# Optimization experiments

Hardware: AMD Instinct MI355X
Metric: run time of the kernel (lower is better)

Reference implementation:

```python
import math
import jax, jax.numpy as jnp
import numpy as np

# ---- SLAYER neuron / simulation constants (from config) ----
THETA = 10.0      # spike threshold
TAU_SR = 10.0     # PSP (SRM) kernel time constant
TAU_REF = 1.0     # refractory kernel time constant
TS = 1.0          # simulation time step
T_SAMPLE = 500    # number of time bins
B, N_IN, N_HID, N_OUT = 64, 1024, 1024, 10


def _alpha_kernel(tau, mult, eps=0.01):
    """slayer _calculateAlphaKernel: mult * t/tau * exp(1 - t/tau), truncated."""
    vals = []
    t = 0.0
    while t < T_SAMPLE:
        v = mult * t / tau * math.exp(1.0 - t / tau)
        if abs(v) < eps and t > tau:
            break
        vals.append(v)
        t += TS
    return np.asarray(vals, np.float32)

SRM_KERNEL = jnp.asarray(_alpha_kernel(TAU_SR, 1.0))            # [K]
REF_KERNEL = jnp.asarray(_alpha_kernel(TAU_REF, -2.0 * THETA))  # [Kr], REF_KERNEL[0] == 0


def dense(x, W):
    # per-timestep fully-connected layer (slayer.dense == 1x1x1 conv3d, no bias)
    # x: [B, Nin, T], W: [Nout, Nin] -> [B, Nout, T]
    return jnp.einsum('oi,bit->bot', W, x)


def psp(x):
    # causal temporal convolution with the SRM kernel: out[t] = Ts * sum_k srm[k] * x[t-k]
    Bx, N, T = x.shape
    K = SRM_KERNEL.shape[0]
    k = SRM_KERNEL[::-1].reshape(1, 1, K).astype(x.dtype)  # flip -> true convolution
    y = jax.lax.conv_general_dilated(
        x.reshape(Bx * N, 1, T), k, (1,), [(K - 1, 0)],
        dimension_numbers=('NCH', 'OIH', 'NCH'))
    return y.reshape(Bx, N, T) * TS


def spike_impl(u_in):
    # sequential LIF thresholding with refractory feedback (slayer spike kernel)
    # u_in: [B, N, T] membrane drive; returns (spikes, membrane) both [B, N, T]
    Kr = REF_KERNEL.shape[0]
    # buf[j] is the refractory contribution arriving at step t+j; new spike at t
    # contributes REF_KERNEL[j] at t+j (REF_KERNEL[0]==0), i.e. shifted kernel into buf.
    refk = jnp.concatenate([REF_KERNEL[1:], jnp.zeros((1,), u_in.dtype)]).astype(u_in.dtype)
    buf0 = jnp.zeros(u_in.shape[:-1] + (Kr,), u_in.dtype)

    def step(buf, u_t):
        u = u_t + buf[..., 0]                              # membrane at time t
        s = (u >= THETA).astype(u_in.dtype) / TS           # spike (amplitude 1/Ts)
        buf = jnp.concatenate([buf[..., 1:], jnp.zeros_like(buf[..., :1])], axis=-1)
        buf = buf + s[..., None] * refk
        return buf, (s, u)

    _, (s, u) = jax.lax.scan(step, buf0, jnp.moveaxis(u_in, -1, 0))
    return jnp.moveaxis(s, 0, -1), jnp.moveaxis(u, 0, -1)


def setup_inputs() -> dict:
    key = jax.random.key(0)
    k1, k2, k3 = jax.random.split(key, 3)
    spike_input = (jax.random.uniform(k1, (B, N_IN, T_SAMPLE)) < 0.05).astype(jnp.float32)
    W1 = jax.random.normal(k2, (N_HID, N_IN), jnp.float32) * 0.3
    W2 = jax.random.normal(k3, (N_OUT, N_HID), jnp.float32) * 0.3
    return {"spike_input": spike_input, "W1": W1, "W2": W2}


def reference(spike_input, W1, W2):
    s1, _ = spike_impl(psp(dense(spike_input, W1)))
    s2, _ = spike_impl(psp(dense(s1, W2)))
    return s2
```

## Files before the change

kernel.cpp:

```cpp
#include <hip/hip_runtime.h>
#include <stdint.h>
#include <math.h>

#define T_SIM 500
#define NB    64
#define NIN   1024
#define NHID  1024
#define NOUT  10
#define KSRM  77
#define CHUNK 32
#define TT5   12
#define NT5   42
#define RING5 128

__device__ __forceinline__ double srm_tap(int k) {
  double u = (double)k / 10.0;
  double v = u * exp(1.0 - u);
  return (double)(float)v;
}
__device__ __forceinline__ double ref_tap(int j) {
  double v = (-20.0 * (double)j) * exp(1.0 - (double)j);
  return (double)(float)v;
}

__global__ __launch_bounds__(64)
void k_pack(const float* __restrict__ x, unsigned long long* __restrict__ bits) {
  const int b = blockIdx.x, ig = blockIdx.y, tc = blockIdx.z;
  const int lane = threadIdx.x;
  const float* xr = x + ((size_t)b * NIN + ig * 64 + lane) * T_SIM;
  const int t0 = tc * 100;
  for (int t = t0; t < t0 + 100; t += 4) {
    const float4 v = *(const float4*)(xr + t);
    unsigned long long m0 = __ballot(v.x > 0.5f);
    unsigned long long m1 = __ballot(v.y > 0.5f);
    unsigned long long m2 = __ballot(v.z > 0.5f);
    unsigned long long m3 = __ballot(v.w > 0.5f);
    if (lane == 0) {
      unsigned long long* w = bits + (size_t)(b * T_SIM + t) * 16 + ig;
      w[0] = m0; w[16] = m1; w[32] = m2; w[48] = m3;
    }
  }
}

__global__ __launch_bounds__(256)
void k_transpose(const float* __restrict__ W1, float* __restrict__ W1T) {
  __shared__ float tile[64][65];
  const int bo = blockIdx.x * 64, bi = blockIdx.y * 64;
  for (int k = threadIdx.x; k < 4096; k += 256) {
    int r = k >> 6, c = k & 63;
    tile[r][c] = W1[(size_t)(bo + r) * NIN + bi + c];
  }
  __syncthreads();
  for (int k = threadIdx.x; k < 4096; k += 256) {
    int r = k >> 6, c = k & 63;
    W1T[(size_t)(bi + r) * NHID + bo + c] = tile[c][r];
  }
}

__global__ __launch_bounds__(128)
void k_dense1(const uint32_t* __restrict__ bits, const float* __restrict__ W1T,
              double* __restrict__ a1c, int col_base) {
  __shared__ int list[NIN];
  __shared__ int nact_s;
  const int col_loc = blockIdx.x;
  const int tid = threadIdx.x;
  if (tid < 32) {
    uint32_t w = bits[(size_t)(col_base + col_loc) * 32 + tid];
    int c = __popc(w);
    int p = c;
#pragma unroll
    for (int d = 1; d < 32; d <<= 1) {
      int q = __shfl_up(p, d);
      if (tid >= d) p += q;
    }
    int excl = p - c;
    while (w) {
      const int j = __ffs(w) - 1;
      w &= w - 1;
      list[excl++] = tid * 32 + j;
    }
    if (tid == 31) nact_s = excl;
  }
  __syncthreads();
  const int n = nact_s;
  const int o = blockIdx.y * 512 + tid * 4;
  double ax[4] = {0,0,0,0}, ay[4] = {0,0,0,0};
  double az[4] = {0,0,0,0}, aw[4] = {0,0,0,0};
  float4 L[8];
  int g = 0;
  if (n >= 8) {
#pragma unroll
    for (int r = 0; r < 8; ++r)
      L[r] = *(const float4*)(W1T + (size_t)list[r] * NHID + o);
    for (g = 0; g + 16 <= n; g += 8) {
      float4 Nb[8];
#pragma unroll
      for (int r = 0; r < 8; ++r)
        Nb[r] = *(const float4*)(W1T + (size_t)list[g + 8 + r] * NHID + o);
#pragma unroll
      for (int r = 0; r < 8; ++r) {
        const int s = r & 3;
        ax[s] += (double)L[r].x; ay[s] += (double)L[r].y;
        az[s] += (double)L[r].z; aw[s] += (double)L[r].w;
      }
#pragma unroll
      for (int r = 0; r < 8; ++r) L[r] = Nb[r];
    }
#pragma unroll
    for (int r = 0; r < 8; ++r) {
      const int s = r & 3;
      ax[s] += (double)L[r].x; ay[s] += (double)L[r].y;
      az[s] += (double)L[r].z; aw[s] += (double)L[r].w;
    }
    g += 8;
  }
  for (; g < n; ++g) {
    const float4 wv = *(const float4*)(W1T + (size_t)list[g] * NHID + o);
    const int s = g & 3;
    ax[s] += (double)wv.x; ay[s] += (double)wv.y;
    az[s] += (double)wv.z; aw[s] += (double)wv.w;
  }
  double* dst = a1c + (size_t)col_loc * NHID + o;
  __builtin_nontemporal_store((ax[0] + ax[1]) + (ax[2] + ax[3]), dst + 0);
  __builtin_nontemporal_store((ay[0] + ay[1]) + (ay[2] + ay[3]), dst + 1);
  __builtin_nontemporal_store((az[0] + az[1]) + (az[2] + az[3]), dst + 2);
  __builtin_nontemporal_store((aw[0] + aw[1]) + (aw[2] + aw[3]), dst + 3);
}

__global__ __launch_bounds__(448)
void k_ps1(const double* __restrict__ a1c, uint32_t* __restrict__ s1w,
           int b_base) {
  __shared__ double S[RING5 * 32];
  __shared__ double Yp[2][4][TT5 * 32];
  __shared__ double TB[80];
  const int ng = blockIdx.x, b_loc = blockIdx.y;
  const int tid = threadIdx.x;
  const double* __restrict__ abase = a1c + (size_t)b_loc * T_SIM * NHID + ng * 32;
  uint32_t* __restrict__ sbase = s1w + (size_t)(b_base + b_loc) * T_SIM * 32 + ng;

  if (tid < 80) TB[tid] = (tid <= 76) ? srm_tap(tid) : 0.0;
  for (int i = tid; i < RING5 * 32; i += 448) S[i] = 0.0;
  __syncthreads();
  for (int id = tid; id < TT5 * 32; id += 448) {
    const int r = id >> 5, nn = id & 31;
    S[r * 32 + nn] = abase[(size_t)r * NHID + nn];
  }

  const bool isFIR = (tid < 384);
  const int g   = tid / 96;
  const int rem = tid - g * 96;
  const int q   = rem >> 5;
  const int n   = rem & 31;
  double tap[20];
  __syncthreads();
  if (isFIR) {
#pragma unroll
    for (int j = 0; j < 20; ++j) tap[j] = TB[20 * g + j];
  }
  double refk[11];
#pragma unroll
  for (int j = 1; j <= 10; ++j) refk[j] = ref_tap(j);
  uint32_t smask = 0;

  for (int k = 0; k < NT5; ++k) {
    const int t0 = k * TT5;
    const int tv = (T_SIM - t0 < TT5) ? (T_SIM - t0) : TT5;
    const int t0n = t0 + TT5;
    const int tvn = (t0n >= T_SIM) ? 0 : ((T_SIM - t0n < TT5) ? (T_SIM - t0n) : TT5);
    if (isFIR) {
      double pf = 0.0;
      const int pr = tid >> 5, pn = tid & 31;
      const bool hasPf = (tid < tvn * 32);
      if (hasPf) pf = abase[(size_t)(t0n + pr) * NHID + pn];
      const int tb = t0 + q * 4;
      int slot = (tb - 20 * g - 19 + 1024) & (RING5 - 1);
      double a0 = 0, a1 = 0, a2 = 0, a3 = 0;
#pragma unroll
      for (int s = 0; s < 23; ++s) {
        const double v = S[slot * 32 + n];
        slot = (slot + 1) & (RING5 - 1);
        if (s <= 19)           a0 += tap[19 - s] * v;
        if (s >= 1 && s <= 20) a1 += tap[20 - s] * v;
        if (s >= 2 && s <= 21) a2 += tap[21 - s] * v;
        if (s >= 3)            a3 += tap[22 - s] * v;
      }
      double* Yk = Yp[k & 1][g];
      const int tl = q * 4;
      if (tl + 0 < tv) Yk[(tl + 0) * 32 + n] = a0;
      if (tl + 1 < tv) Yk[(tl + 1) * 32 + n] = a1;
      if (tl + 2 < tv) Yk[(tl + 2) * 32 + n] = a2;
      if (tl + 3 < tv) Yk[(tl + 3) * 32 + n] = a3;
      if (hasPf) S[((t0n + pr) & (RING5 - 1)) * 32 + pn] = pf;
    } else if (k > 0) {
      const int lane = tid - 384;
      if (lane < 32) {
        const int t0p = t0 - TT5;
        const double* Y0 = Yp[(k - 1) & 1][0];
        const double* Y1 = Yp[(k - 1) & 1][1];
        const double* Y2 = Yp[(k - 1) & 1][2];
        const double* Y3 = Yp[(k - 1) & 1][3];
        for (int gg = 0; gg < TT5; ++gg) {
          double u = (Y0[gg * 32 + lane] + Y1[gg * 32 + lane]) +
                     (Y2[gg * 32 + lane] + Y3[gg * 32 + lane]);
#pragma unroll
          for (int j = 10; j >= 1; --j)
            u += refk[j] * (double)((smask >> (j - 1)) & 1u);
          const bool sp = (u >= 10.0);
          smask = (smask << 1) | (sp ? 1u : 0u);
          const unsigned long long bm = __ballot(sp);
          if (lane == 0) sbase[(size_t)(t0p + gg) * 32] = (uint32_t)bm;
        }
      }
    }
    __syncthreads();
  }
  if (!isFIR) {
    const int lane = tid - 384;
    if (lane < 32) {
      const int t0p = (NT5 - 1) * TT5;
      const int tvp = T_SIM - t0p;
      const double* Y0 = Yp[(NT5 - 1) & 1][0];
      const double* Y1 = Yp[(NT5 - 1) & 1][1];
      const double* Y2 = Yp[(NT5 - 1) & 1][2];
      const double* Y3 = Yp[(NT5 - 1) & 1][3];
      for (int gg = 0; gg < tvp; ++gg) {
        double u = (Y0[gg * 32 + lane] + Y1[gg * 32 + lane]) +
                   (Y2[gg * 32 + lane] + Y3[gg * 32 + lane]);
#pragma unroll
        for (int j = 10; j >= 1; --j)
          u += refk[j] * (double)((smask >> (j - 1)) & 1u);
        const bool sp = (u >= 10.0);
        smask = (smask << 1) | (sp ? 1u : 0u);
        const unsigned long long bm = __ballot(sp);
        if (lane == 0) sbase[(size_t)(t0p + gg) * 32] = (uint32_t)bm;
      }
    }
  }
}

__global__ __launch_bounds__(256)
void k_dense2(const uint32_t* __restrict__ s1w,
              const float* __restrict__ W2, double* __restrict__ a2) {
  __shared__ float w2t[NHID * NOUT];
  for (int k = threadIdx.x; k < NHID * NOUT; k += 256) {
    const int o = k >> 10, i = k & 1023;
    w2t[i * NOUT + o] = W2[k];
  }
  __syncthreads();
  const int col = blockIdx.x * 256 + threadIdx.x;
  double acc[NOUT];
#pragma unroll
  for (int o = 0; o < NOUT; ++o) acc[o] = 0.0;
  const uint32_t* w = s1w + (size_t)col * 32;
  for (int wi = 0; wi < 32; ++wi) {
    uint32_t m = w[wi];
    const int ibase = wi * 32;
    while (m) {
      const int j = __ffs(m) - 1;
      m &= m - 1;
      const float* row = &w2t[(ibase + j) * NOUT];
#pragma unroll
      for (int o = 0; o < NOUT; ++o) acc[o] += (double)row[o];
    }
  }
  double* outp = a2 + (size_t)col * NOUT;
#pragma unroll
  for (int o = 0; o < NOUT; ++o) outp[o] = acc[o];
}

__global__ __launch_bounds__(256)
void k_l2(const double* __restrict__ a2, float* __restrict__ out) {
  __shared__ double S[T_SIM * NOUT];
  __shared__ double Y[T_SIM * NOUT];
  __shared__ double srm[KSRM];
  const int b = blockIdx.x, tid = threadIdx.x;
  if (tid < KSRM) srm[tid] = srm_tap(tid);
  for (int i = tid; i < T_SIM * NOUT; i += 256)
    S[i] = a2[(size_t)b * T_SIM * NOUT + i];
  __syncthreads();
  for (int i = tid; i < T_SIM * NOUT; i += 256) {
    const int t = i / 10, o = i - t * 10;
    const int kmax = (t < KSRM - 1) ? t : (KSRM - 1);
    double acc = 0.0;
    for (int k = 0; k <= kmax; ++k)
      acc += srm[k] * S[(t - k) * 10 + o];
    Y[i] = acc;
  }
  __syncthreads();
  if (tid < NOUT) {
    double refk[11];
#pragma unroll
    for (int j = 1; j <= 10; ++j) refk[j] = ref_tap(j);
    uint32_t smask = 0;
    float* op = out + ((size_t)b * NOUT + tid) * T_SIM;
    for (int t = 0; t < T_SIM; ++t) {
      double u = Y[t * 10 + tid];
#pragma unroll
      for (int j = 10; j >= 1; --j)
        u += refk[j] * (double)((smask >> (j - 1)) & 1u);
      const bool sp = (u >= 10.0);
      smask = (smask << 1) | (sp ? 1u : 0u);
      op[t] = sp ? 1.0f : 0.0f;
    }
  }
}

extern "C" void kernel_launch(void* const* d_in, const int* in_sizes, int n_in,
                              void* d_out, int out_size, void* d_ws, size_t ws_size,
                              hipStream_t stream) {
  const float* x  = (const float*)d_in[0];
  const float* W1 = (const float*)d_in[1];
  const float* W2 = (const float*)d_in[2];
  float* out = (float*)d_out;

  char* ws = (char*)d_ws;
  unsigned long long* bits1 = (unsigned long long*)(ws);
  float*  W1T = (float*) (ws + 4096000);
  double* a1c = (double*)(ws + 8290304);
  uint32_t* s1w = (uint32_t*)(ws + 139362304);
  double* a2  = (double*)(ws + 143458304);

  hipLaunchKernelGGL(k_pack, dim3(NB, 16, 5), dim3(64), 0, stream, x, bits1);
  hipLaunchKernelGGL(k_transpose, dim3(16, 16), dim3(256), 0, stream, W1, W1T);

  for (int bc = 0; bc < NB; bc += CHUNK) {
    hipLaunchKernelGGL(k_dense1, dim3(CHUNK * T_SIM, 2), dim3(128), 0, stream,
                       (const uint32_t*)bits1, W1T, a1c, bc * T_SIM);
    hipLaunchKernelGGL(k_ps1, dim3(32, CHUNK), dim3(448), 0, stream,
                       a1c, s1w, bc);
  }

  hipLaunchKernelGGL(k_dense2, dim3(125), dim3(256), 0, stream, s1w, W2, a2);
  hipLaunchKernelGGL(k_l2, dim3(NB), dim3(256), 0, stream, a2, out);
}
```

Baseline: 935.4 us.

## Tile dense1 through shared memory so W1T rows are reused across 64 columns

Replaces the per-column gather of active W1T rows with a tiled kernel. Each block stages 64-row by 128-output slices of W1T in LDS and processes 64 (batch, time) columns, walking spike bitmasks per 64-input chunk. This reuses each weight load across many columns instead of re-reading rows from L2 per column. In exchange it loads all W1T rows whether or not they are active, and the bit loops diverge across the wave. It also does many LDS reads with fp64 accumulation.

```diff
diff --git a/kernel.cpp b/kernel.cpp
--- a/kernel.cpp
+++ b/kernel.cpp
@@ -57,74 +57,57 @@
   }
 }
 
-__global__ __launch_bounds__(128)
+__global__ __launch_bounds__(512)
 void k_dense1(const uint32_t* __restrict__ bits, const float* __restrict__ W1T,
               double* __restrict__ a1c, int col_base) {
-  __shared__ int list[NIN];
-  __shared__ int nact_s;
-  const int col_loc = blockIdx.x;
+  __shared__ float Wl[64][128];
+  __shared__ uint32_t Lm[64][32];
+  const int ct = blockIdx.x >> 3;
+  const int ot = blockIdx.x & 7;
   const int tid = threadIdx.x;
-  if (tid < 32) {
-    uint32_t w = bits[(size_t)(col_base + col_loc) * 32 + tid];
-    int c = __popc(w);
-    int p = c;
-#pragma unroll
-    for (int d = 1; d < 32; d <<= 1) {
-      int q = __shfl_up(p, d);
-      if (tid >= d) p += q;
-    }
-    int excl = p - c;
-    while (w) {
-      const int j = __ffs(w) - 1;
-      w &= w - 1;
-      list[excl++] = tid * 32 + j;
-    }
-    if (tid == 31) nact_s = excl;
-  }
-  __syncthreads();
-  const int n = nact_s;
-  const int o = blockIdx.y * 512 + tid * 4;
-  double ax[4] = {0,0,0,0}, ay[4] = {0,0,0,0};
-  double az[4] = {0,0,0,0}, aw[4] = {0,0,0,0};
-  float4 L[8];
-  int g = 0;
-  if (n >= 8) {
-#pragma unroll
-    for (int r = 0; r < 8; ++r)
-      L[r] = *(const float4*)(W1T + (size_t)list[r] * NHID + o);
-    for (g = 0; g + 16 <= n; g += 8) {
-      float4 Nb[8];
-#pragma unroll
-      for (int r = 0; r < 8; ++r)
-        Nb[r] = *(const float4*)(W1T + (size_t)list[g + 8 + r] * NHID + o);
-#pragma unroll
-      for (int r = 0; r < 8; ++r) {
-        const int s = r & 3;
-        ax[s] += (double)L[r].x; ay[s] += (double)L[r].y;
-        az[s] += (double)L[r].z; aw[s] += (double)L[r].w;
-      }
-#pragma unroll
-      for (int r = 0; r < 8; ++r) L[r] = Nb[r];
-    }
-#pragma unroll
-    for (int r = 0; r < 8; ++r) {
-      const int s = r & 3;
-      ax[s] += (double)L[r].x; ay[s] += (double)L[r].y;
-      az[s] += (double)L[r].z; aw[s] += (double)L[r].w;
-    }
-    g += 8;
-  }
-  for (; g < n; ++g) {
-    const float4 wv = *(const float4*)(W1T + (size_t)list[g] * NHID + o);
-    const int s = g & 3;
-    ax[s] += (double)wv.x; ay[s] += (double)wv.y;
-    az[s] += (double)wv.z; aw[s] += (double)wv.w;
-  }
-  double* dst = a1c + (size_t)col_loc * NHID + o;
-  __builtin_nontemporal_store((ax[0] + ax[1]) + (ax[2] + ax[3]), dst + 0);
-  __builtin_nontemporal_store((ay[0] + ay[1]) + (ay[2] + ay[3]), dst + 1);
-  __builtin_nontemporal_store((az[0] + az[1]) + (az[2] + az[3]), dst + 2);
-  __builtin_nontemporal_store((aw[0] + aw[1]) + (aw[2] + aw[3]), dst + 3);
+  const int o_l = tid & 127;
+  const int cg  = tid >> 7;
+  const int col0 = ct * 64;
+  const int o0 = ot * 128;
+
+  for (int idx = tid; idx < 64 * 32; idx += 512) {
+    const int c = idx >> 5, w = idx & 31;
+    Lm[c][w] = bits[(size_t)(col_base + col0 + c) * 32 + w];
+  }
+
+  double acc[16];
+#pragma unroll
+  for (int c = 0; c < 16; ++c) acc[c] = 0.0;
+
+  for (int it = 0; it < 16; ++it) {
+    __syncthreads();
+#pragma unroll
+    for (int v = 0; v < 4; ++v) {
+      const int idx = v * 512 + tid;
+      const int row = idx >> 5, c4 = idx & 31;
+      *(float4*)&Wl[row][c4 * 4] =
+          *(const float4*)(W1T + (size_t)(it * 64 + row) * NHID + o0 + c4 * 4);
+    }
+    __syncthreads();
+#pragma unroll
+    for (int c = 0; c < 16; ++c) {
+      uint32_t m0 = Lm[cg * 16 + c][2 * it];
+      uint32_t m1 = Lm[cg * 16 + c][2 * it + 1];
+      while (m0) {
+        const int j = __ffs(m0) - 1; m0 &= m0 - 1;
+        acc[c] += (double)Wl[j][o_l];
+      }
+      while (m1) {
+        const int j = __ffs(m1) - 1; m1 &= m1 - 1;
+        acc[c] += (double)Wl[32 + j][o_l];
+      }
+    }
+  }
+#pragma unroll
+  for (int c = 0; c < 16; ++c) {
+    const int col = col0 + cg * 16 + c;
+    __builtin_nontemporal_store(acc[c], a1c + (size_t)col * NHID + o0 + o_l);
+  }
 }
 
 __global__ __launch_bounds__(448)
@@ -324,7 +307,7 @@
   hipLaunchKernelGGL(k_transpose, dim3(16, 16), dim3(256), 0, stream, W1, W1T);
 
   for (int bc = 0; bc < NB; bc += CHUNK) {
-    hipLaunchKernelGGL(k_dense1, dim3(CHUNK * T_SIM, 2), dim3(128), 0, stream,
+    hipLaunchKernelGGL(k_dense1, dim3(250 * 8), dim3(512), 0, stream,
                        (const uint32_t*)bits1, W1T, a1c, bc * T_SIM);
     hipLaunchKernelGGL(k_ps1, dim3(32, CHUNK), dim3(448), 0, stream,
                        a1c, s1w, bc);
```

After: 1.184 ms. +26.6%, slower.
